# Optimization experiments

Measured on AMD Instinct MI355X. Metric: run time of the kernel, lower is better.

## Reference

```python
import math
import jax, jax.numpy as jnp
import numpy as np

B = 4096
IN_FEATURES = 512
OUT_FEATURES = 1024
SPARSITY = 0.01  # kwta.sparsity
X_DENSITY = 0.1  # fraction of active bits in the binary SDR input


def setup_inputs() -> dict:
    key = jax.random.key(0)
    kx, kw = jax.random.split(key)
    # binary sparse SDR input (the module counts nonzeros, expects sparse binary x)
    x = (jax.random.uniform(kx, (B, IN_FEATURES)) < X_DENSITY).astype(jnp.float32)
    weight = jax.random.normal(kw, (OUT_FEATURES, IN_FEATURES), dtype=jnp.float32)
    return {"x": x, "weight": weight}


def reference(x, weight):
    Bn, in_f = x.shape
    out_f = weight.shape[0]
    k_active = math.ceil(SPARSITY * out_f)   # serial MP steps (11)
    k_in = math.ceil(SPARSITY * in_f)        # kwta winners on xr (6)
    rows = jnp.arange(Bn)

    nonzero = jnp.sum(x != 0, axis=1)
    lambd = (3 * jnp.max(nonzero) * in_f).astype(jnp.float32)

    def wta(r):  # one-hot argmax per row -> binary [B, out_f]
        idx = jnp.argmax(r, axis=1)
        return jnp.zeros_like(r).at[rows, idx].set(1.0)

    def kwta(v):  # binary top-k per row -> binary [B, in_f]
        _, idx = jax.lax.top_k(v, k_in)
        return jnp.zeros_like(v).at[rows[:, None], idx].set(1.0)

    two_x = 2.0 * x
    wT = weight.T  # [in_f, out_f]

    def step(carry, _):
        encoded, xr = carry
        residual = (two_x - xr) @ wT - lambd * encoded      # [B, out_f]
        encoded = encoded + wta(residual)
        xr = kwta(encoded @ weight)                          # [B, in_f]
        return (encoded, xr), None

    init = (jnp.zeros((Bn, out_f), jnp.float32), jnp.zeros_like(x))
    (encoded, xr), _ = jax.lax.scan(step, init, None, length=k_active)
    return encoded, xr
```

## Files before the change

kernel.cpp:

```cpp
#include <hip/hip_runtime.h>

#define IN_F 512
#define OUT_F 1024
#define K_ACTIVE 11
#define K_IN 6

__global__ __launch_bounds__(256) void transpose_w_kernel(const float* __restrict__ w,
                                                          float* __restrict__ wT) {
    __shared__ float tile[32][33];
    const int tx = threadIdx.x & 31;
    const int ty = threadIdx.x >> 5;
    const int i0 = blockIdx.x * 32;
    const int j0 = blockIdx.y * 32;
#pragma unroll
    for (int k = 0; k < 4; ++k)
        tile[ty + 8 * k][tx] = w[(size_t)(j0 + ty + 8 * k) * IN_F + (i0 + tx)];
    __syncthreads();
#pragma unroll
    for (int k = 0; k < 4; ++k)
        wT[(size_t)(i0 + ty + 8 * k) * OUT_F + (j0 + tx)] = tile[tx][ty + 8 * k];
}

__device__ __forceinline__ unsigned long long pack_key(double v, unsigned rev,
                                                       unsigned long long mask) {
    unsigned long long b = (unsigned long long)__double_as_longlong(v);
    unsigned long long m =
        (unsigned long long)((long long)b >> 63) | 0x8000000000000000ull;
    unsigned long long u = b ^ m;
    return (u & ~mask) | (unsigned long long)rev;
}

template <int C>
__device__ __forceinline__ unsigned long long dppmax(unsigned long long k) {
    unsigned lo = (unsigned)__builtin_amdgcn_update_dpp(0, (int)(unsigned)k, C, 0xF, 0xF, true);
    unsigned hi = (unsigned)__builtin_amdgcn_update_dpp(0, (int)(unsigned)(k >> 32), C, 0xF, 0xF, true);
    unsigned long long o = ((unsigned long long)hi << 32) | lo;
    return o > k ? o : k;
}

__device__ __forceinline__ unsigned long long wave_max_u64(unsigned long long k) {
    k = dppmax<0x111>(k);
    k = dppmax<0x112>(k);
    k = dppmax<0x114>(k);
    k = dppmax<0x118>(k);
    k = dppmax<0x142>(k);
    k = dppmax<0x143>(k);
    unsigned glo = (unsigned)__builtin_amdgcn_readlane((int)(unsigned)k, 63);
    unsigned ghi = (unsigned)__builtin_amdgcn_readlane((int)(unsigned)(k >> 32), 63);
    return ((unsigned long long)ghi << 32) | glo;
}

template <bool USE_T>
__device__ __forceinline__ void wt_row_axpy(double* r, const float* __restrict__ wT,
                                            const float* __restrict__ w, int i,
                                            double sgn, int lane) {
    if constexpr (USE_T) {
        const float* rp = wT + ((size_t)i << 10) + (lane << 2);
#pragma unroll
        for (int c = 0; c < 4; ++c) {
            const float4 f = *(const float4*)(rp + (c << 8));
            r[4 * c + 0] += sgn * (double)f.x;
            r[4 * c + 1] += sgn * (double)f.y;
            r[4 * c + 2] += sgn * (double)f.z;
            r[4 * c + 3] += sgn * (double)f.w;
        }
    } else {
#pragma unroll
        for (int s = 0; s < 16; ++s) {
            int j = ((s >> 2) << 8) | (lane << 2) | (s & 3);
            r[s] += sgn * (double)w[(size_t)j * IN_F + i];
        }
    }
}

template <bool USE_T>
__global__ __launch_bounds__(64)
__attribute__((amdgpu_waves_per_eu(4, 4)))
void bmp_kernel(const float* __restrict__ x, const float* __restrict__ w,
                const float* __restrict__ wT, float* __restrict__ out, int rows) {
    __shared__ unsigned short act[IN_F + 8];
    const int lane = threadIdx.x;
    const int row = blockIdx.x;
    if (row >= rows) return;

    const float* xrow = x + (size_t)row * IN_F;
    int cnt = 0;
#pragma unroll
    for (int c = 0; c < IN_F / 64; ++c) {
        bool pbit = xrow[c * 64 + lane] != 0.0f;
        unsigned long long m = __ballot(pbit);
        int pre = __popcll(m & ((1ull << lane) - 1ull));
        if (pbit) act[cnt + pre] = (unsigned short)(c * 64 + lane);
        cnt += __popcll(m);
    }
    __syncthreads();

    double r[16];
#pragma unroll
    for (int s = 0; s < 16; ++s) r[s] = 0.0;
    {
        int iu = act[0];
#pragma unroll 1
        for (int k = 0; k < cnt; ++k) {
            int inx = act[k + 1];
            wt_row_axpy<USE_T>(r, wT, w, iu, 1.0, lane);
            iu = inx;
        }
    }
#pragma unroll
    for (int s = 0; s < 16; ++s) r[s] *= 2.0;

    double vd[8];
#pragma unroll
    for (int p = 0; p < 8; ++p) vd[p] = 0.0;

    unsigned enc = 0;
    unsigned selmask = 0;
    int O0 = -1, O1 = -1, O2 = -1, O3 = -1, O4 = -1, O5 = -1;

#pragma unroll 1
    for (int t = 0; t < K_ACTIVE; ++t) {
        unsigned long long kb = 0;
#pragma unroll
        for (int s = 0; s < 16; ++s) {
            int j = ((s >> 2) << 8) | (lane << 2) | (s & 3);
            unsigned long long key = pack_key(r[s], 1023u ^ (unsigned)j, 1023ull);
            key = (enc & (1u << s)) ? 0ull : key;
            kb = key > kb ? key : kb;
        }
        const unsigned long long g = wave_max_u64(kb);
        const int bestj = 1023 ^ (int)(g & 1023ull);
        if (lane == ((bestj >> 2) & 63))
            enc |= 1u << ((((bestj >> 8) & 3) << 2) | (bestj & 3));

        {
            const float* wr = w + ((size_t)bestj << 9) + (lane << 2);
#pragma unroll
            for (int c = 0; c < 2; ++c) {
                const float4 f = *(const float4*)(wr + (c << 8));
                vd[4 * c + 0] += (double)f.x;
                vd[4 * c + 1] += (double)f.y;
                vd[4 * c + 2] += (double)f.z;
                vd[4 * c + 3] += (double)f.w;
            }
        }

        int N[6];
        {
            unsigned long long vkey[8];
#pragma unroll
            for (int p = 0; p < 8; ++p) {
                int i = ((p >> 2) << 8) | (lane << 2) | (p & 3);
                vkey[p] = pack_key(vd[p], 511u ^ (unsigned)i, 511ull);
            }
#pragma unroll
            for (int s2 = 0; s2 < K_IN; ++s2) {
                unsigned long long lk = vkey[0];
#pragma unroll
                for (int p = 1; p < 8; ++p) lk = vkey[p] > lk ? vkey[p] : lk;
                const unsigned long long gk = wave_max_u64(lk);
                N[s2] = 511 ^ (int)(gk & 511ull);
#pragma unroll
                for (int p = 0; p < 8; ++p) vkey[p] = (vkey[p] == gk) ? 0ull : vkey[p];
            }
            if (t == K_ACTIVE - 1) {
                selmask = 0;
#pragma unroll
                for (int p = 0; p < 8; ++p) selmask |= (vkey[p] == 0ull) ? (1u << p) : 0u;
            }
        }

        if (t == 0) {
#pragma unroll
            for (int b = 0; b < 6; ++b) wt_row_axpy<USE_T>(r, wT, w, N[b], -1.0, lane);
        } else if (t < K_ACTIVE - 1) {
#pragma unroll
            for (int a = 0; a < 6; ++a) {
                const int o = (a == 0) ? O0 : (a == 1) ? O1 : (a == 2) ? O2
                              : (a == 3) ? O3 : (a == 4) ? O4 : O5;
                const bool stay = (o == N[0]) | (o == N[1]) | (o == N[2]) |
                                  (o == N[3]) | (o == N[4]) | (o == N[5]);
                if (!stay) wt_row_axpy<USE_T>(r, wT, w, o, 1.0, lane);
            }
#pragma unroll
            for (int b = 0; b < 6; ++b) {
                const int n = N[b];
                const bool was = (n == O0) | (n == O1) | (n == O2) |
                                 (n == O3) | (n == O4) | (n == O5);
                if (!was) wt_row_axpy<USE_T>(r, wT, w, n, -1.0, lane);
            }
        }
        O0 = N[0]; O1 = N[1]; O2 = N[2]; O3 = N[3]; O4 = N[4]; O5 = N[5];
    }

    float* oe = out + (size_t)row * OUT_F + (lane << 2);
#pragma unroll
    for (int c = 0; c < 4; ++c) {
        float4 v;
        v.x = (enc & (1u << (4 * c + 0))) ? 1.0f : 0.0f;
        v.y = (enc & (1u << (4 * c + 1))) ? 1.0f : 0.0f;
        v.z = (enc & (1u << (4 * c + 2))) ? 1.0f : 0.0f;
        v.w = (enc & (1u << (4 * c + 3))) ? 1.0f : 0.0f;
        *(float4*)(oe + (c << 8)) = v;
    }
    float* ox = out + (size_t)rows * OUT_F + (size_t)row * IN_F + (lane << 2);
#pragma unroll
    for (int c = 0; c < 2; ++c) {
        float4 v;
        v.x = (selmask & (1u << (4 * c + 0))) ? 1.0f : 0.0f;
        v.y = (selmask & (1u << (4 * c + 1))) ? 1.0f : 0.0f;
        v.z = (selmask & (1u << (4 * c + 2))) ? 1.0f : 0.0f;
        v.w = (selmask & (1u << (4 * c + 3))) ? 1.0f : 0.0f;
        *(float4*)(ox + (c << 8)) = v;
    }
}

extern "C" void kernel_launch(void* const* d_in, const int* in_sizes, int n_in,
                              void* d_out, int out_size, void* d_ws, size_t ws_size,
                              hipStream_t stream) {
    const float* x = (const float*)d_in[0];
    const float* w = (const float*)d_in[1];
    float* out = (float*)d_out;
    const int rows = in_sizes[0] / IN_F;

    const size_t wt_bytes = (size_t)IN_F * OUT_F * sizeof(float);
    if (ws_size >= wt_bytes && d_ws != nullptr) {
        float* wT = (float*)d_ws;
        transpose_w_kernel<<<dim3(IN_F / 32, OUT_F / 32), 256, 0, stream>>>(w, wT);
        bmp_kernel<true><<<rows, 64, 0, stream>>>(x, w, wT, out, rows);
    } else {
        bmp_kernel<false><<<rows, 64, 0, stream>>>(x, w, nullptr, out, rows);
    }
}
```

Baseline: 168.6 us.

## Split matching pursuit across two waves with pairwise gathers and 32-bit reductions

```diff
diff --git a/kernel.cpp b/kernel.cpp
--- a/kernel.cpp
+++ b/kernel.cpp
@@ -20,6 +20,9 @@
     for (int k = 0; k < 4; ++k)
         wT[(size_t)(i0 + ty + 8 * k) * OUT_F + (j0 + tx)] = tile[tx][ty + 8 * k];
 }
+__global__ void zero_row_f_kernel(float* __restrict__ wT) {
+    wT[(size_t)IN_F * OUT_F + blockIdx.x * 256 + threadIdx.x] = 0.0f;
+}
 
 __device__ __forceinline__ unsigned long long pack_key(double v, unsigned rev,
                                                        unsigned long long mask) {
@@ -31,55 +34,88 @@
 }
 
 template <int C>
-__device__ __forceinline__ unsigned long long dppmax(unsigned long long k) {
-    unsigned lo = (unsigned)__builtin_amdgcn_update_dpp(0, (int)(unsigned)k, C, 0xF, 0xF, true);
-    unsigned hi = (unsigned)__builtin_amdgcn_update_dpp(0, (int)(unsigned)(k >> 32), C, 0xF, 0xF, true);
-    unsigned long long o = ((unsigned long long)hi << 32) | lo;
-    return o > k ? o : k;
-}
-
-__device__ __forceinline__ unsigned long long wave_max_u64(unsigned long long k) {
-    k = dppmax<0x111>(k);
-    k = dppmax<0x112>(k);
-    k = dppmax<0x114>(k);
-    k = dppmax<0x118>(k);
-    k = dppmax<0x142>(k);
-    k = dppmax<0x143>(k);
-    unsigned glo = (unsigned)__builtin_amdgcn_readlane((int)(unsigned)k, 63);
-    unsigned ghi = (unsigned)__builtin_amdgcn_readlane((int)(unsigned)(k >> 32), 63);
-    return ((unsigned long long)ghi << 32) | glo;
-}
-
-template <bool USE_T>
-__device__ __forceinline__ void wt_row_axpy(double* r, const float* __restrict__ wT,
-                                            const float* __restrict__ w, int i,
-                                            double sgn, int lane) {
-    if constexpr (USE_T) {
-        const float* rp = wT + ((size_t)i << 10) + (lane << 2);
-#pragma unroll
-        for (int c = 0; c < 4; ++c) {
-            const float4 f = *(const float4*)(rp + (c << 8));
-            r[4 * c + 0] += sgn * (double)f.x;
-            r[4 * c + 1] += sgn * (double)f.y;
-            r[4 * c + 2] += sgn * (double)f.z;
-            r[4 * c + 3] += sgn * (double)f.w;
-        }
+__device__ __forceinline__ unsigned maxdpp(unsigned v) {
+    unsigned t = (unsigned)__builtin_amdgcn_update_dpp(0, (int)v, C, 0xF, 0xF, true);
+    return t > v ? t : v;
+}
+__device__ __forceinline__ unsigned wave_umax(unsigned v) {
+    v = maxdpp<0x111>(v);
+    v = maxdpp<0x112>(v);
+    v = maxdpp<0x114>(v);
+    v = maxdpp<0x118>(v);
+    v = maxdpp<0x142>(v);
+    v = maxdpp<0x143>(v);
+    return (unsigned)__builtin_amdgcn_readlane((int)v, 63);
+}
+
+__device__ __forceinline__ unsigned long long wave_max_key(unsigned long long k) {
+    const unsigned h = (unsigned)(k >> 32), l = (unsigned)k;
+    const unsigned gh = wave_umax(h);
+    const unsigned long long tied = __ballot(h == gh);
+    unsigned gl;
+    if (__popcll(tied) == 1) {
+        gl = (unsigned)__builtin_amdgcn_readlane((int)l,
+                                                 (int)__ffsll((long long)tied) - 1);
     } else {
-#pragma unroll
-        for (int s = 0; s < 16; ++s) {
-            int j = ((s >> 2) << 8) | (lane << 2) | (s & 3);
-            r[s] += sgn * (double)w[(size_t)j * IN_F + i];
-        }
-    }
-}
-
-template <bool USE_T>
-__global__ __launch_bounds__(64)
-__attribute__((amdgpu_waves_per_eu(4, 4)))
-void bmp_kernel(const float* __restrict__ x, const float* __restrict__ w,
-                const float* __restrict__ wT, float* __restrict__ out, int rows) {
+        gl = wave_umax((h == gh) ? l : 0u);
+    }
+    return ((unsigned long long)gh << 32) | gl;
+}
+
+__device__ __forceinline__ void half_add2(double* rh, const float* __restrict__ wT,
+                                          int i0, int i1, int lane, int wv) {
+    const float* p0 = wT + ((size_t)i0 << 10) + (wv << 9) + (lane << 2);
+    const float* p1 = wT + ((size_t)i1 << 10) + (wv << 9) + (lane << 2);
+    const float4 f0 = *(const float4*)(p0);
+    const float4 f1 = *(const float4*)(p0 + 256);
+    const float4 g0 = *(const float4*)(p1);
+    const float4 g1 = *(const float4*)(p1 + 256);
+    rh[0] += (double)f0.x + (double)g0.x;  rh[1] += (double)f0.y + (double)g0.y;
+    rh[2] += (double)f0.z + (double)g0.z;  rh[3] += (double)f0.w + (double)g0.w;
+    rh[4] += (double)f1.x + (double)g1.x;  rh[5] += (double)f1.y + (double)g1.y;
+    rh[6] += (double)f1.z + (double)g1.z;  rh[7] += (double)f1.w + (double)g1.w;
+}
+
+__device__ __forceinline__ void full_axpy(double* r, const float* __restrict__ wT,
+                                          int i, double sgn, int lane) {
+    const float* rp = wT + ((size_t)i << 10) + (lane << 2);
+#pragma unroll
+    for (int C = 0; C < 4; ++C) {
+        const float4 f = *(const float4*)(rp + (C << 8));
+        r[4 * C + 0] += sgn * (double)f.x;
+        r[4 * C + 1] += sgn * (double)f.y;
+        r[4 * C + 2] += sgn * (double)f.z;
+        r[4 * C + 3] += sgn * (double)f.w;
+    }
+}
+
+__device__ __forceinline__ void half_add0(double* rh, const float* __restrict__ w,
+                                          int i, int lane, int wv) {
+#pragma unroll
+    for (int s = 0; s < 8; ++s) {
+        const int j = (wv << 9) | ((s >> 2) << 8) | (lane << 2) | (s & 3);
+        rh[s] += (double)w[(size_t)j * IN_F + i];
+    }
+}
+__device__ __forceinline__ void full_axpy0(double* r, const float* __restrict__ w,
+                                           int i, double sgn, int lane) {
+#pragma unroll
+    for (int S = 0; S < 16; ++S) {
+        const int j = ((S >> 2) << 8) | (lane << 2) | (S & 3);
+        r[S] += sgn * (double)w[(size_t)j * IN_F + i];
+    }
+}
+
+template <int MODE>
+__global__ __launch_bounds__(128) void bmp_kernel(const float* __restrict__ x,
+                                                  const float* __restrict__ w,
+                                                  const float* __restrict__ wT,
+                                                  float* __restrict__ out, int rows) {
     __shared__ unsigned short act[IN_F + 8];
-    const int lane = threadIdx.x;
+    __shared__ double rxfer[IN_F];
+    __shared__ int msg[8];
+    const int lane = threadIdx.x & 63;
+    const int wv = threadIdx.x >> 6;
     const int row = blockIdx.x;
     if (row >= rows) return;
 
@@ -90,29 +126,38 @@
         bool pbit = xrow[c * 64 + lane] != 0.0f;
         unsigned long long m = __ballot(pbit);
         int pre = __popcll(m & ((1ull << lane) - 1ull));
-        if (pbit) act[cnt + pre] = (unsigned short)(c * 64 + lane);
+        if (wv == 0 && pbit) act[cnt + pre] = (unsigned short)(c * 64 + lane);
         cnt += __popcll(m);
     }
+    if (wv == 0 && lane < 2) act[cnt + lane] = (unsigned short)IN_F;
     __syncthreads();
 
-    double r[16];
-#pragma unroll
-    for (int s = 0; s < 16; ++s) r[s] = 0.0;
+    double st[16];
+#pragma unroll
+    for (int s = 0; s < 16; ++s) st[s] = 0.0;
+
     {
-        int iu = act[0];
+        double* rh = st + (wv << 3);
+        if constexpr (MODE == 1) {
 #pragma unroll 1
-        for (int k = 0; k < cnt; ++k) {
-            int inx = act[k + 1];
-            wt_row_axpy<USE_T>(r, wT, w, iu, 1.0, lane);
-            iu = inx;
-        }
-    }
-#pragma unroll
-    for (int s = 0; s < 16; ++s) r[s] *= 2.0;
-
-    double vd[8];
-#pragma unroll
-    for (int p = 0; p < 8; ++p) vd[p] = 0.0;
+            for (int k = 0; k < cnt; k += 2)
+                half_add2(rh, wT, act[k], act[k + 1], lane, wv);
+        } else {
+#pragma unroll 1
+            for (int k = 0; k < cnt; ++k) half_add0(rh, w, act[k], lane, wv);
+        }
+#pragma unroll
+        for (int s = 0; s < 8; ++s) rh[s] *= 2.0;
+    }
+    if (wv == 1) {
+#pragma unroll
+        for (int s = 0; s < 8; ++s) rxfer[s * 64 + lane] = st[8 + s];
+    }
+    __syncthreads();
+    if (wv == 0) {
+#pragma unroll
+        for (int s = 0; s < 8; ++s) st[8 + s] = rxfer[s * 64 + lane];
+    }
 
     unsigned enc = 0;
     unsigned selmask = 0;
@@ -120,98 +165,138 @@
 
 #pragma unroll 1
     for (int t = 0; t < K_ACTIVE; ++t) {
-        unsigned long long kb = 0;
-#pragma unroll
-        for (int s = 0; s < 16; ++s) {
-            int j = ((s >> 2) << 8) | (lane << 2) | (s & 3);
-            unsigned long long key = pack_key(r[s], 1023u ^ (unsigned)j, 1023ull);
-            key = (enc & (1u << s)) ? 0ull : key;
-            kb = key > kb ? key : kb;
-        }
-        const unsigned long long g = wave_max_u64(kb);
-        const int bestj = 1023 ^ (int)(g & 1023ull);
-        if (lane == ((bestj >> 2) & 63))
-            enc |= 1u << ((((bestj >> 8) & 3) << 2) | (bestj & 3));
-
-        {
+        if (wv == 0) {
+            unsigned long long kb = 0;
+#pragma unroll
+            for (int S = 0; S < 16; ++S) {
+                const int j = ((S >> 2) << 8) | (lane << 2) | (S & 3);
+                unsigned long long key = pack_key(st[S], 1023u ^ (unsigned)j, 1023ull);
+                key = (enc & (1u << S)) ? 0ull : key;
+                kb = key > kb ? key : kb;
+            }
+            const unsigned long long g = wave_max_key(kb);
+            const int bestj = 1023 ^ (int)(g & 1023ull);
+            if (((bestj >> 2) & 63) == lane)
+                enc |= 1u << ((((bestj >> 8) & 3) << 2) | (bestj & 3));
+            if (lane == 0) msg[0] = bestj;
+        }
+        __syncthreads();
+        if (wv == 1) {
+            const int bestj = __builtin_amdgcn_readfirstlane(msg[0]);
             const float* wr = w + ((size_t)bestj << 9) + (lane << 2);
-#pragma unroll
-            for (int c = 0; c < 2; ++c) {
-                const float4 f = *(const float4*)(wr + (c << 8));
-                vd[4 * c + 0] += (double)f.x;
-                vd[4 * c + 1] += (double)f.y;
-                vd[4 * c + 2] += (double)f.z;
-                vd[4 * c + 3] += (double)f.w;
-            }
-        }
-
-        int N[6];
-        {
-            unsigned long long vkey[8];
+            {
+                const float4 f0 = *(const float4*)wr;
+                const float4 f1 = *(const float4*)(wr + 256);
+                st[0] += (double)f0.x;  st[1] += (double)f0.y;
+                st[2] += (double)f0.z;  st[3] += (double)f0.w;
+                st[4] += (double)f1.x;  st[5] += (double)f1.y;
+                st[6] += (double)f1.z;  st[7] += (double)f1.w;
+            }
 #pragma unroll
             for (int p = 0; p < 8; ++p) {
-                int i = ((p >> 2) << 8) | (lane << 2) | (p & 3);
-                vkey[p] = pack_key(vd[p], 511u ^ (unsigned)i, 511ull);
+                const int i = ((p >> 2) << 8) | (lane << 2) | (p & 3);
+                st[8 + p] = __longlong_as_double(
+                    (long long)pack_key(st[p], 511u ^ (unsigned)i, 511ull));
             }
 #pragma unroll
             for (int s2 = 0; s2 < K_IN; ++s2) {
-                unsigned long long lk = vkey[0];
-#pragma unroll
-                for (int p = 1; p < 8; ++p) lk = vkey[p] > lk ? vkey[p] : lk;
-                const unsigned long long gk = wave_max_u64(lk);
-                N[s2] = 511 ^ (int)(gk & 511ull);
-#pragma unroll
-                for (int p = 0; p < 8; ++p) vkey[p] = (vkey[p] == gk) ? 0ull : vkey[p];
+                unsigned long long lk = (unsigned long long)__double_as_longlong(st[8]);
+#pragma unroll
+                for (int p = 1; p < 8; ++p) {
+                    const unsigned long long kk =
+                        (unsigned long long)__double_as_longlong(st[8 + p]);
+                    lk = kk > lk ? kk : lk;
+                }
+                const unsigned long long gk = wave_max_key(lk);
+                if (lane == 0) msg[1 + s2] = 511 ^ (int)(gk & 511ull);
+#pragma unroll
+                for (int p = 0; p < 8; ++p) {
+                    const unsigned long long kk =
+                        (unsigned long long)__double_as_longlong(st[8 + p]);
+                    st[8 + p] = __longlong_as_double((long long)(kk == gk ? 0ull : kk));
+                }
             }
             if (t == K_ACTIVE - 1) {
                 selmask = 0;
 #pragma unroll
-                for (int p = 0; p < 8; ++p) selmask |= (vkey[p] == 0ull) ? (1u << p) : 0u;
-            }
-        }
-
-        if (t == 0) {
-#pragma unroll
-            for (int b = 0; b < 6; ++b) wt_row_axpy<USE_T>(r, wT, w, N[b], -1.0, lane);
-        } else if (t < K_ACTIVE - 1) {
-#pragma unroll
-            for (int a = 0; a < 6; ++a) {
-                const int o = (a == 0) ? O0 : (a == 1) ? O1 : (a == 2) ? O2
-                              : (a == 3) ? O3 : (a == 4) ? O4 : O5;
-                const bool stay = (o == N[0]) | (o == N[1]) | (o == N[2]) |
-                                  (o == N[3]) | (o == N[4]) | (o == N[5]);
-                if (!stay) wt_row_axpy<USE_T>(r, wT, w, o, 1.0, lane);
-            }
-#pragma unroll
-            for (int b = 0; b < 6; ++b) {
-                const int n = N[b];
-                const bool was = (n == O0) | (n == O1) | (n == O2) |
-                                 (n == O3) | (n == O4) | (n == O5);
-                if (!was) wt_row_axpy<USE_T>(r, wT, w, n, -1.0, lane);
-            }
-        }
-        O0 = N[0]; O1 = N[1]; O2 = N[2]; O3 = N[3]; O4 = N[4]; O5 = N[5];
-    }
-
-    float* oe = out + (size_t)row * OUT_F + (lane << 2);
-#pragma unroll
-    for (int c = 0; c < 4; ++c) {
-        float4 v;
-        v.x = (enc & (1u << (4 * c + 0))) ? 1.0f : 0.0f;
-        v.y = (enc & (1u << (4 * c + 1))) ? 1.0f : 0.0f;
-        v.z = (enc & (1u << (4 * c + 2))) ? 1.0f : 0.0f;
-        v.w = (enc & (1u << (4 * c + 3))) ? 1.0f : 0.0f;
-        *(float4*)(oe + (c << 8)) = v;
-    }
-    float* ox = out + (size_t)rows * OUT_F + (size_t)row * IN_F + (lane << 2);
-#pragma unroll
-    for (int c = 0; c < 2; ++c) {
-        float4 v;
-        v.x = (selmask & (1u << (4 * c + 0))) ? 1.0f : 0.0f;
-        v.y = (selmask & (1u << (4 * c + 1))) ? 1.0f : 0.0f;
-        v.z = (selmask & (1u << (4 * c + 2))) ? 1.0f : 0.0f;
-        v.w = (selmask & (1u << (4 * c + 3))) ? 1.0f : 0.0f;
-        *(float4*)(ox + (c << 8)) = v;
+                for (int p = 0; p < 8; ++p)
+                    selmask |= (__double_as_longlong(st[8 + p]) == 0ll) ? (1u << p) : 0u;
+            }
+        }
+        __syncthreads();
+        if (wv == 0 && t < K_ACTIVE - 1) {
+            const int N0 = __builtin_amdgcn_readfirstlane(msg[1]);
+            const int N1 = __builtin_amdgcn_readfirstlane(msg[2]);
+            const int N2 = __builtin_amdgcn_readfirstlane(msg[3]);
+            const int N3 = __builtin_amdgcn_readfirstlane(msg[4]);
+            const int N4 = __builtin_amdgcn_readfirstlane(msg[5]);
+            const int N5 = __builtin_amdgcn_readfirstlane(msg[6]);
+            if (t == 0) {
+                if constexpr (MODE == 1) {
+                    full_axpy(st, wT, N0, -1.0, lane);
+                    full_axpy(st, wT, N1, -1.0, lane);
+                    full_axpy(st, wT, N2, -1.0, lane);
+                    full_axpy(st, wT, N3, -1.0, lane);
+                    full_axpy(st, wT, N4, -1.0, lane);
+                    full_axpy(st, wT, N5, -1.0, lane);
+                } else {
+                    full_axpy0(st, w, N0, -1.0, lane);
+                    full_axpy0(st, w, N1, -1.0, lane);
+                    full_axpy0(st, w, N2, -1.0, lane);
+                    full_axpy0(st, w, N3, -1.0, lane);
+                    full_axpy0(st, w, N4, -1.0, lane);
+                    full_axpy0(st, w, N5, -1.0, lane);
+                }
+            } else {
+#pragma unroll
+                for (int a = 0; a < 6; ++a) {
+                    const int o = (a == 0) ? O0 : (a == 1) ? O1 : (a == 2) ? O2
+                                  : (a == 3) ? O3 : (a == 4) ? O4 : O5;
+                    const bool stay = (o == N0) | (o == N1) | (o == N2) |
+                                      (o == N3) | (o == N4) | (o == N5);
+                    if (!stay) {
+                        if constexpr (MODE == 1) full_axpy(st, wT, o, 1.0, lane);
+                        else full_axpy0(st, w, o, 1.0, lane);
+                    }
+                }
+#pragma unroll
+                for (int b = 0; b < 6; ++b) {
+                    const int n = (b == 0) ? N0 : (b == 1) ? N1 : (b == 2) ? N2
+                                  : (b == 3) ? N3 : (b == 4) ? N4 : N5;
+                    const bool was = (n == O0) | (n == O1) | (n == O2) |
+                                     (n == O3) | (n == O4) | (n == O5);
+                    if (!was) {
+                        if constexpr (MODE == 1) full_axpy(st, wT, n, -1.0, lane);
+                        else full_axpy0(st, w, n, -1.0, lane);
+                    }
+                }
+            }
+            O0 = N0; O1 = N1; O2 = N2; O3 = N3; O4 = N4; O5 = N5;
+        }
+    }
+
+    if (wv == 0) {
+        float* oe = out + (size_t)row * OUT_F + (lane << 2);
+#pragma unroll
+        for (int C = 0; C < 4; ++C) {
+            float4 v;
+            v.x = (enc & (1u << (4 * C + 0))) ? 1.0f : 0.0f;
+            v.y = (enc & (1u << (4 * C + 1))) ? 1.0f : 0.0f;
+            v.z = (enc & (1u << (4 * C + 2))) ? 1.0f : 0.0f;
+            v.w = (enc & (1u << (4 * C + 3))) ? 1.0f : 0.0f;
+            *(float4*)(oe + (C << 8)) = v;
+        }
+    } else {
+        float* ox = out + (size_t)rows * OUT_F + (size_t)row * IN_F + (lane << 2);
+#pragma unroll
+        for (int c = 0; c < 2; ++c) {
+            float4 v;
+            v.x = (selmask & (1u << (4 * c + 0))) ? 1.0f : 0.0f;
+            v.y = (selmask & (1u << (4 * c + 1))) ? 1.0f : 0.0f;
+            v.z = (selmask & (1u << (4 * c + 2))) ? 1.0f : 0.0f;
+            v.w = (selmask & (1u << (4 * c + 3))) ? 1.0f : 0.0f;
+            *(float4*)(ox + (c << 8)) = v;
+        }
     }
 }
 
@@ -223,12 +308,14 @@
     float* out = (float*)d_out;
     const int rows = in_sizes[0] / IN_F;
 
-    const size_t wt_bytes = (size_t)IN_F * OUT_F * sizeof(float);
-    if (ws_size >= wt_bytes && d_ws != nullptr) {
+    const size_t need_f = (size_t)(IN_F + 1) * OUT_F * sizeof(float);
+
+    if (d_ws != nullptr && ws_size >= need_f) {
         float* wT = (float*)d_ws;
         transpose_w_kernel<<<dim3(IN_F / 32, OUT_F / 32), 256, 0, stream>>>(w, wT);
-        bmp_kernel<true><<<rows, 64, 0, stream>>>(x, w, wT, out, rows);
+        zero_row_f_kernel<<<OUT_F / 256, 256, 0, stream>>>(wT);
+        bmp_kernel<1><<<rows, 128, 0, stream>>>(x, w, wT, out, rows);
     } else {
-        bmp_kernel<false><<<rows, 64, 0, stream>>>(x, w, nullptr, out, rows);
-    }
-}
+        bmp_kernel<0><<<rows, 128, 0, stream>>>(x, w, nullptr, out, rows);
+    }
+}
```

Result: slower. 552.5 us (+227.6%).

## Use 32-bit high-word argmax with tie fallback, ballot-driven input loop, two rows per block

Applied to the files above, without the earlier changes.

```diff
diff --git a/kernel.cpp b/kernel.cpp
--- a/kernel.cpp
+++ b/kernel.cpp
@@ -30,31 +30,45 @@
     return (u & ~mask) | (unsigned long long)rev;
 }
 
+__device__ __forceinline__ unsigned hi_key(double v) {
+    const int hi = __double2hiint(v);
+    return (unsigned)hi ^ ((unsigned)(hi >> 31) | 0x80000000u);
+}
+
 template <int C>
-__device__ __forceinline__ unsigned long long dppmax(unsigned long long k) {
-    unsigned lo = (unsigned)__builtin_amdgcn_update_dpp(0, (int)(unsigned)k, C, 0xF, 0xF, true);
-    unsigned hi = (unsigned)__builtin_amdgcn_update_dpp(0, (int)(unsigned)(k >> 32), C, 0xF, 0xF, true);
-    unsigned long long o = ((unsigned long long)hi << 32) | lo;
-    return o > k ? o : k;
-}
-
-__device__ __forceinline__ unsigned long long wave_max_u64(unsigned long long k) {
-    k = dppmax<0x111>(k);
-    k = dppmax<0x112>(k);
-    k = dppmax<0x114>(k);
-    k = dppmax<0x118>(k);
-    k = dppmax<0x142>(k);
-    k = dppmax<0x143>(k);
-    unsigned glo = (unsigned)__builtin_amdgcn_readlane((int)(unsigned)k, 63);
-    unsigned ghi = (unsigned)__builtin_amdgcn_readlane((int)(unsigned)(k >> 32), 63);
-    return ((unsigned long long)ghi << 32) | glo;
-}
-
-template <bool USE_T>
-__device__ __forceinline__ void wt_row_axpy(double* r, const float* __restrict__ wT,
-                                            const float* __restrict__ w, int i,
-                                            double sgn, int lane) {
-    if constexpr (USE_T) {
+__device__ __forceinline__ unsigned maxdpp(unsigned v) {
+    unsigned t = (unsigned)__builtin_amdgcn_update_dpp(0, (int)v, C, 0xF, 0xF, true);
+    return t > v ? t : v;
+}
+__device__ __forceinline__ unsigned wave_umax(unsigned v) {
+    v = maxdpp<0x111>(v);
+    v = maxdpp<0x112>(v);
+    v = maxdpp<0x114>(v);
+    v = maxdpp<0x118>(v);
+    v = maxdpp<0x142>(v);
+    v = maxdpp<0x143>(v);
+    return (unsigned)__builtin_amdgcn_readlane((int)v, 63);
+}
+
+__device__ __forceinline__ unsigned long long wave_max_key(unsigned long long k) {
+    const unsigned h = (unsigned)(k >> 32), l = (unsigned)k;
+    const unsigned gh = wave_umax(h);
+    const unsigned long long tied = __ballot(h == gh);
+    unsigned gl;
+    if (__popcll(tied) == 1) {
+        gl = (unsigned)__builtin_amdgcn_readlane((int)l,
+                                                 (int)__ffsll((long long)tied) - 1);
+    } else {
+        gl = wave_umax((h == gh) ? l : 0u);
+    }
+    return ((unsigned long long)gh << 32) | gl;
+}
+
+template <int MODE>
+__device__ __forceinline__ void full_axpy(double* r, const float* __restrict__ wT,
+                                          const float* __restrict__ w, int i,
+                                          double sgn, int lane) {
+    if constexpr (MODE == 1) {
         const float* rp = wT + ((size_t)i << 10) + (lane << 2);
 #pragma unroll
         for (int c = 0; c < 4; ++c) {
@@ -66,49 +80,40 @@
         }
     } else {
 #pragma unroll
-        for (int s = 0; s < 16; ++s) {
-            int j = ((s >> 2) << 8) | (lane << 2) | (s & 3);
-            r[s] += sgn * (double)w[(size_t)j * IN_F + i];
-        }
-    }
-}
-
-template <bool USE_T>
-__global__ __launch_bounds__(64)
-__attribute__((amdgpu_waves_per_eu(4, 4)))
-void bmp_kernel(const float* __restrict__ x, const float* __restrict__ w,
-                const float* __restrict__ wT, float* __restrict__ out, int rows) {
-    __shared__ unsigned short act[IN_F + 8];
-    const int lane = threadIdx.x;
-    const int row = blockIdx.x;
+        for (int S = 0; S < 16; ++S) {
+            const int j = ((S >> 2) << 8) | (lane << 2) | (S & 3);
+            r[S] += sgn * (double)w[(size_t)j * IN_F + i];
+        }
+    }
+}
+
+template <int MODE>
+__global__ __launch_bounds__(128) void bmp_kernel(const float* __restrict__ x,
+                                                  const float* __restrict__ w,
+                                                  const float* __restrict__ wT,
+                                                  float* __restrict__ out, int rows) {
+    const int lane = threadIdx.x & 63;
+    const int row = blockIdx.x * 2 + (threadIdx.x >> 6);
     if (row >= rows) return;
 
-    const float* xrow = x + (size_t)row * IN_F;
-    int cnt = 0;
-#pragma unroll
-    for (int c = 0; c < IN_F / 64; ++c) {
-        bool pbit = xrow[c * 64 + lane] != 0.0f;
-        unsigned long long m = __ballot(pbit);
-        int pre = __popcll(m & ((1ull << lane) - 1ull));
-        if (pbit) act[cnt + pre] = (unsigned short)(c * 64 + lane);
-        cnt += __popcll(m);
-    }
-    __syncthreads();
-
     double r[16];
 #pragma unroll
-    for (int s = 0; s < 16; ++s) r[s] = 0.0;
+    for (int S = 0; S < 16; ++S) r[S] = 0.0;
     {
-        int iu = act[0];
+        const float* xrow = x + (size_t)row * IN_F;
 #pragma unroll 1
-        for (int k = 0; k < cnt; ++k) {
-            int inx = act[k + 1];
-            wt_row_axpy<USE_T>(r, wT, w, iu, 1.0, lane);
-            iu = inx;
-        }
-    }
-#pragma unroll
-    for (int s = 0; s < 16; ++s) r[s] *= 2.0;
+        for (int c = 0; c < IN_F / 64; ++c) {
+            const float xv = xrow[c * 64 + lane];
+            unsigned long long m = __ballot(xv != 0.0f);
+            while (m) {
+                const int b = (int)__ffsll((long long)m) - 1;
+                m &= m - 1;
+                full_axpy<MODE>(r, wT, w, c * 64 + b, 1.0, lane);
+            }
+        }
+    }
+#pragma unroll
+    for (int S = 0; S < 16; ++S) r[S] *= 2.0;
 
     double vd[8];
 #pragma unroll
@@ -120,74 +125,120 @@
 
 #pragma unroll 1
     for (int t = 0; t < K_ACTIVE; ++t) {
-        unsigned long long kb = 0;
-#pragma unroll
-        for (int s = 0; s < 16; ++s) {
-            int j = ((s >> 2) << 8) | (lane << 2) | (s & 3);
-            unsigned long long key = pack_key(r[s], 1023u ^ (unsigned)j, 1023ull);
-            key = (enc & (1u << s)) ? 0ull : key;
-            kb = key > kb ? key : kb;
-        }
-        const unsigned long long g = wave_max_u64(kb);
-        const int bestj = 1023 ^ (int)(g & 1023ull);
-        if (lane == ((bestj >> 2) & 63))
+        unsigned lv = 0;
+#pragma unroll
+        for (int S = 0; S < 16; ++S) {
+            const unsigned key = hi_key(r[S]);
+            lv = ((enc >> S) & 1u) ? lv : (key > lv ? key : lv);
+        }
+        const unsigned g = wave_umax(lv);
+        const unsigned long long tied = __ballot(lv == g);
+        unsigned mm = 0;
+#pragma unroll
+        for (int S = 0; S < 16; ++S)
+            mm |= (!((enc >> S) & 1u) && hi_key(r[S]) == g) ? (1u << S) : 0u;
+        const int L = (int)__ffsll((long long)tied) - 1;
+        const unsigned mmL = (unsigned)__builtin_amdgcn_readlane((int)mm, L);
+        int bestj;
+        if (__builtin_expect((__popcll(tied) == 1) && !(mmL & (mmL - 1)), 1)) {
+            const int S = __ffs(mmL) - 1;
+            bestj = ((S >> 2) << 8) | (L << 2) | (S & 3);
+        } else {
+            unsigned long long kb = 0;
+#pragma unroll
+            for (int S = 0; S < 16; ++S) {
+                const int j = ((S >> 2) << 8) | (lane << 2) | (S & 3);
+                const unsigned long long fk =
+                    pack_key(r[S], 1023u ^ (unsigned)j, 1023ull);
+                const bool cand = !((enc >> S) & 1u) && hi_key(r[S]) == g;
+                kb = (cand && fk > kb) ? fk : kb;
+            }
+            const unsigned long long gk = wave_max_key(kb);
+            bestj = 1023 ^ (int)(gk & 1023ull);
+        }
+        bestj = __builtin_amdgcn_readfirstlane(bestj);
+        if (((bestj >> 2) & 63) == lane)
             enc |= 1u << ((((bestj >> 8) & 3) << 2) | (bestj & 3));
 
         {
             const float* wr = w + ((size_t)bestj << 9) + (lane << 2);
-#pragma unroll
-            for (int c = 0; c < 2; ++c) {
-                const float4 f = *(const float4*)(wr + (c << 8));
-                vd[4 * c + 0] += (double)f.x;
-                vd[4 * c + 1] += (double)f.y;
-                vd[4 * c + 2] += (double)f.z;
-                vd[4 * c + 3] += (double)f.w;
-            }
+            const float4 f0 = *(const float4*)wr;
+            const float4 f1 = *(const float4*)(wr + 256);
+            vd[0] += (double)f0.x;  vd[1] += (double)f0.y;
+            vd[2] += (double)f0.z;  vd[3] += (double)f0.w;
+            vd[4] += (double)f1.x;  vd[5] += (double)f1.y;
+            vd[6] += (double)f1.z;  vd[7] += (double)f1.w;
         }
 
         int N[6];
         {
-            unsigned long long vkey[8];
-#pragma unroll
-            for (int p = 0; p < 8; ++p) {
-                int i = ((p >> 2) << 8) | (lane << 2) | (p & 3);
-                vkey[p] = pack_key(vd[p], 511u ^ (unsigned)i, 511ull);
-            }
+            unsigned kk[8];
+#pragma unroll
+            for (int p = 0; p < 8; ++p) kk[p] = hi_key(vd[p]);
 #pragma unroll
             for (int s2 = 0; s2 < K_IN; ++s2) {
-                unsigned long long lk = vkey[0];
-#pragma unroll
-                for (int p = 1; p < 8; ++p) lk = vkey[p] > lk ? vkey[p] : lk;
-                const unsigned long long gk = wave_max_u64(lk);
-                N[s2] = 511 ^ (int)(gk & 511ull);
-#pragma unroll
-                for (int p = 0; p < 8; ++p) vkey[p] = (vkey[p] == gk) ? 0ull : vkey[p];
+                unsigned lm = kk[0];
+#pragma unroll
+                for (int p = 1; p < 8; ++p) lm = kk[p] > lm ? kk[p] : lm;
+                const unsigned g2 = wave_umax(lm);
+                const unsigned long long tied2 = __ballot(lm == g2);
+                unsigned mm2 = 0;
+#pragma unroll
+                for (int p = 0; p < 8; ++p) mm2 |= (kk[p] == g2) ? (1u << p) : 0u;
+                const int L2 = (int)__ffsll((long long)tied2) - 1;
+                const unsigned mmL2 =
+                    (unsigned)__builtin_amdgcn_readlane((int)mm2, L2);
+                int n;
+                if (__builtin_expect((__popcll(tied2) == 1) && !(mmL2 & (mmL2 - 1)),
+                                     1)) {
+                    const int bp = __ffs(mmL2) - 1;
+                    n = ((bp >> 2) << 8) | (L2 << 2) | (bp & 3);
+#pragma unroll
+                    for (int p = 0; p < 8; ++p) kk[p] = (kk[p] == g2) ? 0u : kk[p];
+                } else {
+                    unsigned long long kb = 0;
+#pragma unroll
+                    for (int p = 0; p < 8; ++p) {
+                        const int i = ((p >> 2) << 8) | (lane << 2) | (p & 3);
+                        const unsigned long long fk =
+                            pack_key(vd[p], 511u ^ (unsigned)i, 511ull);
+                        kb = (kk[p] == g2 && fk > kb) ? fk : kb;
+                    }
+                    const unsigned long long gk = wave_max_key(kb);
+                    n = 511 ^ (int)(gk & 511ull);
+                    const int ln = (n >> 2) & 63;
+                    const int bp = (((n >> 8) & 1) << 2) | (n & 3);
+#pragma unroll
+                    for (int p = 0; p < 8; ++p)
+                        kk[p] = (lane == ln && p == bp) ? 0u : kk[p];
+                }
+                N[s2] = __builtin_amdgcn_readfirstlane(n);
             }
             if (t == K_ACTIVE - 1) {
                 selmask = 0;
 #pragma unroll
-                for (int p = 0; p < 8; ++p) selmask |= (vkey[p] == 0ull) ? (1u << p) : 0u;
+                for (int p = 0; p < 8; ++p) selmask |= (kk[p] == 0u) ? (1u << p) : 0u;
             }
         }
 
         if (t == 0) {
 #pragma unroll
-            for (int b = 0; b < 6; ++b) wt_row_axpy<USE_T>(r, wT, w, N[b], -1.0, lane);
+            for (int b = 0; b < 6; ++b) full_axpy<MODE>(r, wT, w, N[b], -1.0, lane);
         } else if (t < K_ACTIVE - 1) {
 #pragma unroll
-            for (int a = 0; a < 6; ++a) {
-                const int o = (a == 0) ? O0 : (a == 1) ? O1 : (a == 2) ? O2
-                              : (a == 3) ? O3 : (a == 4) ? O4 : O5;
+            for (int a2 = 0; a2 < 6; ++a2) {
+                const int o = (a2 == 0) ? O0 : (a2 == 1) ? O1 : (a2 == 2) ? O2
+                              : (a2 == 3) ? O3 : (a2 == 4) ? O4 : O5;
                 const bool stay = (o == N[0]) | (o == N[1]) | (o == N[2]) |
                                   (o == N[3]) | (o == N[4]) | (o == N[5]);
-                if (!stay) wt_row_axpy<USE_T>(r, wT, w, o, 1.0, lane);
-            }
-#pragma unroll
-            for (int b = 0; b < 6; ++b) {
-                const int n = N[b];
+                if (!stay) full_axpy<MODE>(r, wT, w, o, 1.0, lane);
+            }
+#pragma unroll
+            for (int b2 = 0; b2 < 6; ++b2) {
+                const int n = N[b2];
                 const bool was = (n == O0) | (n == O1) | (n == O2) |
                                  (n == O3) | (n == O4) | (n == O5);
-                if (!was) wt_row_axpy<USE_T>(r, wT, w, n, -1.0, lane);
+                if (!was) full_axpy<MODE>(r, wT, w, n, -1.0, lane);
             }
         }
         O0 = N[0]; O1 = N[1]; O2 = N[2]; O3 = N[3]; O4 = N[4]; O5 = N[5];
@@ -223,12 +274,14 @@
     float* out = (float*)d_out;
     const int rows = in_sizes[0] / IN_F;
 
-    const size_t wt_bytes = (size_t)IN_F * OUT_F * sizeof(float);
-    if (ws_size >= wt_bytes && d_ws != nullptr) {
+    const size_t need_f = (size_t)IN_F * OUT_F * sizeof(float);
+    const int blocks = (rows + 1) / 2;
+
+    if (d_ws != nullptr && ws_size >= need_f) {
         float* wT = (float*)d_ws;
         transpose_w_kernel<<<dim3(IN_F / 32, OUT_F / 32), 256, 0, stream>>>(w, wT);
-        bmp_kernel<true><<<rows, 64, 0, stream>>>(x, w, wT, out, rows);
+        bmp_kernel<1><<<blocks, 128, 0, stream>>>(x, w, wT, out, rows);
     } else {
-        bmp_kernel<false><<<rows, 64, 0, stream>>>(x, w, nullptr, out, rows);
-    }
-}
+        bmp_kernel<0><<<blocks, 128, 0, stream>>>(x, w, nullptr, out, rows);
+    }
+}
```

Result: slower. 176.4 us (+4.6%).
